# Performance work log

Hardware: AMD Instinct MI355X
Metric: run time of the kernel (lower is better)

Reference implementation:

```python
import jax, jax.numpy as jnp
import numpy as np

B, T = 8, 30000
DIM = 3
HID = 128          # hidden_dim
CD = 128           # c_dim
R = 64             # plane_resolution
NB = 5             # n_blocks


def setup_inputs() -> dict:
    key = jax.random.key(0)
    ks = jax.random.split(key, 10)
    points = jax.random.uniform(ks[0], (B, T, DIM), dtype=jnp.float32)
    index_xz = jax.random.randint(ks[1], (B, T), 0, R * R, dtype=jnp.int32)
    index_xy = jax.random.randint(ks[2], (B, T), 0, R * R, dtype=jnp.int32)
    index_yz = jax.random.randint(ks[3], (B, T), 0, R * R, dtype=jnp.int32)
    s_in = 1.0 / np.sqrt(DIM)
    s_h2 = 1.0 / np.sqrt(2 * HID)
    s_h = 1.0 / np.sqrt(HID)
    fc_pos_w = jax.random.normal(ks[4], (DIM, 2 * HID), jnp.float32) * s_in
    fc_pos_b = jnp.zeros((2 * HID,), jnp.float32)
    fc0_w = jax.random.normal(ks[5], (NB, 2 * HID, HID), jnp.float32) * s_h2
    fc0_b = jnp.zeros((NB, HID), jnp.float32)
    fc1_w = jax.random.normal(ks[6], (NB, HID, HID), jnp.float32) * s_h
    fc1_b = jnp.zeros((NB, HID), jnp.float32)
    sc_w = jax.random.normal(ks[7], (NB, 2 * HID, HID), jnp.float32) * s_h2
    fc_c_w = jax.random.normal(ks[8], (HID, CD), jnp.float32) * s_h
    fc_c_b = jnp.zeros((CD,), jnp.float32)
    return dict(points=points, index_xz=index_xz, index_xy=index_xy, index_yz=index_yz,
                fc_pos_w=fc_pos_w, fc_pos_b=fc_pos_b, fc0_w=fc0_w, fc0_b=fc0_b,
                fc1_w=fc1_w, fc1_b=fc1_b, sc_w=sc_w, fc_c_w=fc_c_w, fc_c_b=fc_c_b)


def _resnet_block(x, w0, b0, w1, b1, ws):
    # ResnetBlockFC: fc_0(relu(x)) -> fc_1(relu(net)); shortcut is bias-free Linear
    net = jax.nn.relu(x) @ w0 + b0
    dx = jax.nn.relu(net) @ w1 + b1
    return x @ ws + dx


def _pool_max_gather(feat, idx):
    # scatter_max per batch into R*R bins, then gather back per-point
    def per(f, i):  # f: [T, C], i: [T]
        seg = jax.ops.segment_max(f, i, num_segments=R * R)  # [R2, C]
        return seg[i]
    return jax.vmap(per)(feat, idx)


def _plane_mean(c, idx):
    # scatter_mean of c [B, T, CD] into [B, CD, R, R] plane features
    def per(f, i):
        s = jax.ops.segment_sum(f, i, num_segments=R * R)  # [R2, CD]
        cnt = jax.ops.segment_sum(jnp.ones((f.shape[0],), f.dtype), i, num_segments=R * R)
        return s / jnp.maximum(cnt, 1.0)[:, None]
    m = jax.vmap(per)(c, idx)  # [B, R2, CD]
    return jnp.transpose(m, (0, 2, 1)).reshape(c.shape[0], CD, R, R)


def reference(points, index_xz, index_xy, index_yz, fc_pos_w, fc_pos_b,
              fc0_w, fc0_b, fc1_w, fc1_b, sc_w, fc_c_w, fc_c_b):
    idxs = (index_xz, index_xy, index_yz)
    net = points @ fc_pos_w + fc_pos_b                    # [B, T, 2*HID]
    net = _resnet_block(net, fc0_w[0], fc0_b[0], fc1_w[0], fc1_b[0], sc_w[0])  # [B, T, HID]
    for i in range(1, NB):
        pooled = sum(_pool_max_gather(net, idx) for idx in idxs)  # pool_local sums over plane keys
        net = jnp.concatenate([net, pooled], axis=2)      # [B, T, 2*HID]
        net = _resnet_block(net, fc0_w[i], fc0_b[i], fc1_w[i], fc1_b[i], sc_w[i])
    c = net @ fc_c_w + fc_c_b                             # [B, T, CD]
    # fea dict {'xz','xy','yz'} returned as a stacked array [3, B, CD, R, R]
    return jnp.stack([_plane_mean(c, index_xz), _plane_mean(c, index_xy), _plane_mean(c, index_yz)], axis=0)
```

## Files before the change

### kernel.cpp

```cpp
#include <hip/hip_runtime.h>
#include <float.h>

#define BATCH 8
#define TPTS 30000
#define NPR 30016
#define HID 128
#define R2 4096
#define NPTS (BATCH * TPTS)
#define PB 64
#define XS 264
#define HS 136

typedef __attribute__((ext_vector_type(8))) short short8;
typedef __attribute__((ext_vector_type(4))) short short4v;
typedef __attribute__((ext_vector_type(4))) float f32x4;

__device__ __forceinline__ short f2bf(float f) {
    unsigned u = __float_as_uint(f);
    u += 0x7fff + ((u >> 16) & 1);
    return (short)(u >> 16);
}
__device__ __forceinline__ float bf2f(unsigned short u) {
    return __uint_as_float(((unsigned)u) << 16);
}
__device__ __forceinline__ unsigned relu2(unsigned u) {
    unsigned sm = u & 0x80008000u;
    unsigned d  = sm - (sm >> 15);
    return u & ~d;
}
__device__ __forceinline__ short8 relu8(short8 v) {
    union { short8 s; unsigned u[4]; } a;
    a.s = v;
#pragma unroll
    for (int i = 0; i < 4; ++i) a.u[i] = relu2(a.u[i]);
    return a.s;
}

__global__ void k_fill4(float4* p, float v, int n4) {
    int i = blockIdx.x * blockDim.x + threadIdx.x;
    if (i < n4) p[i] = make_float4(v, v, v, v);
}

__global__ __launch_bounds__(256) void k_prep(
    const float* __restrict__ fc0w, const float* __restrict__ fc1w, const float* __restrict__ scw,
    const float* __restrict__ fccw,
    short* __restrict__ Wt0, short* __restrict__ Wts, short* __restrict__ Wt1,
    short* __restrict__ Wtc)
{
    int i = blockIdx.x * 256 + threadIdx.x;
    if (i < 5 * 128 * 256) {
        int r = i >> 15;
        int c = (i >> 8) & 127;
        int k = i & 255;
        Wt0[i] = f2bf(fc0w[(r * 256 + k) * 128 + c]);
        Wts[i] = f2bf(scw [(r * 256 + k) * 128 + c]);
    }
    if (i < 5 * 128 * 128) {
        int r = i >> 14;
        int c = (i >> 7) & 127;
        int k = i & 127;
        Wt1[i] = f2bf(fc1w[(r * 128 + k) * 128 + c]);
    }
    if (i < 128 * 128) {
        int c = (i >> 7) & 127;
        int k = i & 127;
        Wtc[i] = f2bf(fccw[k * 128 + c]);
    }
}

__global__ void k_hist(const int* __restrict__ i0, const int* __restrict__ i1,
                       const int* __restrict__ i2, int* __restrict__ hist)
{
    int t = blockIdx.x * 256 + threadIdx.x;
    if (t >= NPTS) return;
    int b = t / TPTS;
    atomicAdd(&hist[(0 * BATCH + b) * R2 + i0[t]], 1);
    atomicAdd(&hist[(1 * BATCH + b) * R2 + i1[t]], 1);
    atomicAdd(&hist[(2 * BATCH + b) * R2 + i2[t]], 1);
}

__global__ __launch_bounds__(256) void k_scan(const int* __restrict__ hist,
                                              int* __restrict__ starts, int* __restrict__ cursor)
{
    int pb = blockIdx.x;
    const int* h = hist + pb * R2;
    int tid = threadIdx.x;
    __shared__ int part[257];
    int loc[16]; int s = 0;
    int base = tid * 16;
#pragma unroll
    for (int q = 0; q < 16; ++q) { loc[q] = s; s += h[base + q]; }
    part[tid + 1] = s;
    __syncthreads();
    if (tid == 0) {
        part[0] = 0;
        for (int i = 1; i <= 256; ++i) part[i] += part[i - 1];
    }
    __syncthreads();
    int off = part[tid];
#pragma unroll
    for (int q = 0; q < 16; ++q) {
        int v = off + loc[q];
        starts[pb * 4097 + base + q] = v;
        cursor[pb * R2 + base + q] = v;
    }
    if (tid == 255) starts[pb * 4097 + 4096] = part[256];
}

__global__ void k_scatter(const int* __restrict__ i0, const int* __restrict__ i1,
                          const int* __restrict__ i2, int* __restrict__ cursor,
                          unsigned short* __restrict__ order)
{
    int t = blockIdx.x * 256 + threadIdx.x;
    if (t >= NPTS) return;
    int b = t / TPTS;
    int tt = t - b * TPTS;
    int s0 = atomicAdd(&cursor[(0 * BATCH + b) * R2 + i0[t]], 1);
    order[(0 * BATCH + b) * TPTS + s0] = (unsigned short)tt;
    int s1 = atomicAdd(&cursor[(1 * BATCH + b) * R2 + i1[t]], 1);
    order[(1 * BATCH + b) * TPTS + s1] = (unsigned short)tt;
    int s2 = atomicAdd(&cursor[(2 * BATCH + b) * R2 + i2[t]], 1);
    order[(2 * BATCH + b) * TPTS + s2] = (unsigned short)tt;
}

__global__ __launch_bounds__(256) void k_poolmax(
    const short* __restrict__ net, const int* __restrict__ starts,
    const unsigned short* __restrict__ order, short* __restrict__ seg)
{
    int b = blockIdx.x;
    int plane = blockIdx.y >> 10;
    int bin = (blockIdx.y & 1023) * 4 + (threadIdx.x >> 6);
    int pb = plane * BATCH + b;
    int lane = threadIdx.x & 63;
    int s = starts[pb * 4097 + bin], e = starts[pb * 4097 + bin + 1];
    if (s == e) return;
    const unsigned short* ord = order + pb * TPTS;
    float vx = -FLT_MAX, vy = -FLT_MAX;
    for (int i = s; i < e; ++i) {
        int t = b * NPR + ord[i];
        unsigned u = *(const unsigned*)(net + t * HID + lane * 2);
        vx = fmaxf(vx, bf2f((unsigned short)(u & 0xFFFF)));
        vy = fmaxf(vy, bf2f((unsigned short)(u >> 16)));
    }
    unsigned o = ((unsigned short)f2bf(vx)) | (((unsigned)(unsigned short)f2bf(vy)) << 16);
    *(unsigned*)(seg + (pb * R2 + bin) * HID + lane * 2) = o;
}

__global__ __launch_bounds__(256) void k_poolmean(
    const short* __restrict__ net, const int* __restrict__ starts,
    const unsigned short* __restrict__ order, short* __restrict__ meanb)
{
    int b = blockIdx.x;
    int plane = blockIdx.y >> 10;
    int bin = (blockIdx.y & 1023) * 4 + (threadIdx.x >> 6);
    int pb = plane * BATCH + b;
    int lane = threadIdx.x & 63;
    int s = starts[pb * 4097 + bin], e = starts[pb * 4097 + bin + 1];
    const unsigned short* ord = order + pb * TPTS;
    float vx = 0.f, vy = 0.f;
    for (int i = s; i < e; ++i) {
        int t = b * NPR + ord[i];
        unsigned u = *(const unsigned*)(net + t * HID + lane * 2);
        vx += bf2f((unsigned short)(u & 0xFFFF));
        vy += bf2f((unsigned short)(u >> 16));
    }
    float inv = 1.f / fmaxf((float)(e - s), 1.f);
    unsigned o = ((unsigned short)f2bf(vx * inv)) | (((unsigned)(unsigned short)f2bf(vy * inv)) << 16);
    *(unsigned*)(meanb + (pb * R2 + bin) * HID + lane * 2) = o;
}

__device__ __forceinline__ void resnet_body(
    short* xs, const float* b0s, const float* b1s,
    const short* __restrict__ Wt0r, const short* __restrict__ Wtsr,
    const short* __restrict__ Wt1r, short* __restrict__ net_out, int t0)
{
    int tid = threadIdx.x;
    int lane = tid & 63;
    int wave = tid >> 6;
    int n    = lane & 15;
    int quad = lane >> 4;
    int ch0  = wave * 32;

    f32x4 accS[2][4] = {};
    f32x4 accF[2][4] = {};
    for (int ks = 0; ks < 8; ++ks) {
        int ko = ks * 32 + quad * 8;
        short8 aS[2], aF[2];
#pragma unroll
        for (int c = 0; c < 2; ++c) {
            int row = ch0 + c * 16 + n;
            aS[c] = *(const short8*)(Wtsr + row * 256 + ko);
            aF[c] = *(const short8*)(Wt0r + row * 256 + ko);
        }
#pragma unroll
        for (int p = 0; p < 4; ++p) {
            short8 bX = *(const short8*)(xs + (p * 16 + n) * XS + ko);
            short8 bR = relu8(bX);
#pragma unroll
            for (int c = 0; c < 2; ++c) {
                accS[c][p] = __builtin_amdgcn_mfma_f32_16x16x32_bf16(aS[c], bX, accS[c][p], 0, 0, 0);
                accF[c][p] = __builtin_amdgcn_mfma_f32_16x16x32_bf16(aF[c], bR, accF[c][p], 0, 0, 0);
            }
        }
    }
    __syncthreads();

    short* h = xs;
#pragma unroll
    for (int c = 0; c < 2; ++c) {
        int chb = ch0 + c * 16 + quad * 4;
#pragma unroll
        for (int p = 0; p < 4; ++p) {
            int pt = p * 16 + n;
            short4v hv;
#pragma unroll
            for (int r = 0; r < 4; ++r)
                hv[r] = f2bf(fmaxf(accF[c][p][r] + b0s[chb + r], 0.f));
            *(short4v*)&h[pt * HS + chb] = hv;
        }
    }
    __syncthreads();

    for (int ks = 0; ks < 4; ++ks) {
        int ko = ks * 32 + quad * 8;
        short8 a1[2];
#pragma unroll
        for (int c = 0; c < 2; ++c)
            a1[c] = *(const short8*)(Wt1r + (ch0 + c * 16 + n) * 128 + ko);
#pragma unroll
        for (int p = 0; p < 4; ++p) {
            short8 bh = *(const short8*)&h[(p * 16 + n) * HS + ko];
#pragma unroll
            for (int c = 0; c < 2; ++c)
                accS[c][p] = __builtin_amdgcn_mfma_f32_16x16x32_bf16(a1[c], bh, accS[c][p], 0, 0, 0);
        }
    }
    __syncthreads();

#pragma unroll
    for (int c = 0; c < 2; ++c) {
        int chb = ch0 + c * 16 + quad * 4;
#pragma unroll
        for (int p = 0; p < 4; ++p) {
            int pt = p * 16 + n;
            short4v o;
#pragma unroll
            for (int r = 0; r < 4; ++r)
                o[r] = f2bf(accS[c][p][r] + b1s[chb + r]);
            *(short4v*)&h[pt * HS + chb] = o;
        }
    }
    __syncthreads();

    int pr = tid >> 4, l8 = (tid & 15) * 8;
#pragma unroll
    for (int it = 0; it < 4; ++it) {
        int p = it * 16 + pr;
        *(short8*)(net_out + (t0 + p) * HID + l8) = *(const short8*)&h[p * HS + l8];
    }
}

__global__ __launch_bounds__(256, 4) void k_mblock0(
    const float* __restrict__ pts, const float* __restrict__ Wp, const float* __restrict__ bp,
    const short* __restrict__ Wt0, const short* __restrict__ Wts, const short* __restrict__ Wt1,
    const float* __restrict__ b0, const float* __restrict__ b1, short* __restrict__ net)
{
    __shared__ short xs[PB * XS];
    __shared__ float b0s[HID], b1s[HID];
    int tid = threadIdx.x;
    int b  = blockIdx.x;
    int r0 = blockIdx.y * PB;
    if (tid < 128) { b0s[tid] = b0[tid]; b1s[tid] = b1[tid]; }

    int j = tid & 127, half = tid >> 7;
    int col = half * 128 + j;
    float w0 = Wp[col], w1 = Wp[256 + col], w2 = Wp[512 + col];
    float bb = bp[col];
    for (int p = 0; p < PB; ++p) {
        int tt = r0 + p; if (tt > TPTS - 1) tt = TPTS - 1;
        const float* pp = pts + (b * TPTS + tt) * 3;
        float v = fmaf(pp[2], w2, fmaf(pp[1], w1, fmaf(pp[0], w0, bb)));
        xs[p * XS + col] = f2bf(v);
    }
    __syncthreads();
    resnet_body(xs, b0s, b1s, Wt0, Wts, Wt1, net, b * NPR + r0);
}

__global__ __launch_bounds__(256, 4) void k_mblock(
    const short* __restrict__ net_in, const short* __restrict__ seg,
    const int* __restrict__ i0, const int* __restrict__ i1, const int* __restrict__ i2,
    const short* __restrict__ Wt0, const short* __restrict__ Wts, const short* __restrict__ Wt1,
    const float* __restrict__ b0, const float* __restrict__ b1, short* __restrict__ net_out)
{
    __shared__ short xs[PB * XS];
    __shared__ float b0s[HID], b1s[HID];
    int tid = threadIdx.x;
    int b  = blockIdx.x;
    int r0 = blockIdx.y * PB;
    if (tid < 128) { b0s[tid] = b0[tid]; b1s[tid] = b1[tid]; }

    int pr = tid >> 4;
    int l8 = (tid & 15) * 8;
#pragma unroll
    for (int it = 0; it < 4; ++it) {
        int p = it * 16 + pr;
        int tt = r0 + p;
        int ttc = tt > TPTS - 1 ? TPTS - 1 : tt;
        int ib = b * TPTS + ttc;
        int a0 = i0[ib], a1 = i1[ib], a2 = i2[ib];
        *(short8*)&xs[p * XS + l8] = *(const short8*)(net_in + (b * NPR + tt) * HID + l8);
        short8 s0 = *(const short8*)(seg + ((0 * BATCH + b) * R2 + a0) * HID + l8);
        short8 s1 = *(const short8*)(seg + ((1 * BATCH + b) * R2 + a1) * HID + l8);
        short8 s2 = *(const short8*)(seg + ((2 * BATCH + b) * R2 + a2) * HID + l8);
        short8 pv;
#pragma unroll
        for (int r = 0; r < 8; ++r)
            pv[r] = f2bf(bf2f((unsigned short)s0[r]) + bf2f((unsigned short)s1[r]) + bf2f((unsigned short)s2[r]));
        *(short8*)&xs[p * XS + 128 + l8] = pv;
    }
    __syncthreads();
    resnet_body(xs, b0s, b1s, Wt0, Wts, Wt1, net_out, b * NPR + r0);
}

__global__ __launch_bounds__(256) void k_gemmout(
    const short* __restrict__ meanb, const short* __restrict__ Wtc, const float* __restrict__ bc,
    const int* __restrict__ starts, float* __restrict__ out)
{
    __shared__ short bs[64 * HS];
    __shared__ float tile[128 * 66];
    __shared__ float bcs[HID];
    __shared__ int   flg[64];
    int tid = threadIdx.x;
    int b = blockIdx.x;
    int plane = blockIdx.y >> 6;
    int pb = plane * BATCH + b;
    int bin0 = (blockIdx.y & 63) * 64;

    if (tid < 128) bcs[tid] = bc[tid];
    if (tid < 64)  flg[tid] = (starts[pb * 4097 + bin0 + tid + 1] > starts[pb * 4097 + bin0 + tid]);
    for (int c8 = tid; c8 < 1024; c8 += 256) {
        int p = c8 >> 4, l = (c8 & 15) * 8;
        *(short8*)&bs[p * HS + l] = *(const short8*)(meanb + (pb * R2 + bin0 + p) * HID + l);
    }
    __syncthreads();

    int lane = tid & 63, wave = tid >> 6;
    int n = lane & 15, quad = lane >> 4;
    int ch0 = wave * 32;
    f32x4 acc[2][4] = {};
    for (int ks = 0; ks < 4; ++ks) {
        int ko = ks * 32 + quad * 8;
        short8 a[2];
#pragma unroll
        for (int c = 0; c < 2; ++c)
            a[c] = *(const short8*)(Wtc + (ch0 + c * 16 + n) * 128 + ko);
#pragma unroll
        for (int p = 0; p < 4; ++p) {
            short8 bh = *(const short8*)&bs[(p * 16 + n) * HS + ko];
#pragma unroll
            for (int c = 0; c < 2; ++c)
                acc[c][p] = __builtin_amdgcn_mfma_f32_16x16x32_bf16(a[c], bh, acc[c][p], 0, 0, 0);
        }
    }
#pragma unroll
    for (int c = 0; c < 2; ++c) {
        int chb = ch0 + c * 16 + quad * 4;
#pragma unroll
        for (int p = 0; p < 4; ++p) {
            int bin = p * 16 + n;
#pragma unroll
            for (int r = 0; r < 4; ++r)
                tile[(chb + r) * 66 + bin] = acc[c][p][r] + bcs[chb + r];
        }
    }
    __syncthreads();

    for (int c4 = tid; c4 < 2048; c4 += 256) {
        int ch = c4 >> 4, b4 = (c4 & 15) * 4;
        float4 o;
        o.x = flg[b4 + 0] ? tile[ch * 66 + b4 + 0] : 0.f;
        o.y = flg[b4 + 1] ? tile[ch * 66 + b4 + 1] : 0.f;
        o.z = flg[b4 + 2] ? tile[ch * 66 + b4 + 2] : 0.f;
        o.w = flg[b4 + 3] ? tile[ch * 66 + b4 + 3] : 0.f;
        *(float4*)(out + (pb * 128 + ch) * R2 + bin0 + b4) = o;
    }
}

extern "C" void kernel_launch(void* const* d_in, const int* in_sizes, int n_in,
                              void* d_out, int out_size, void* d_ws, size_t ws_size,
                              hipStream_t stream) {
    const float* pts  = (const float*)d_in[0];
    const int*   ixz  = (const int*)d_in[1];
    const int*   ixy  = (const int*)d_in[2];
    const int*   iyz  = (const int*)d_in[3];
    const float* Wp   = (const float*)d_in[4];
    const float* bp   = (const float*)d_in[5];
    const float* fc0w = (const float*)d_in[6];
    const float* fc0b = (const float*)d_in[7];
    const float* fc1w = (const float*)d_in[8];
    const float* fc1b = (const float*)d_in[9];
    const float* scw  = (const float*)d_in[10];
    const float* Wc   = (const float*)d_in[11];
    const float* bc   = (const float*)d_in[12];
    float* out = (float*)d_out;

    short* Wt0 = (short*)d_ws;
    short* Wts = Wt0 + 163840;
    short* Wt1 = Wts + 163840;
    short* Wtc = Wt1 + 81920;
    short* net  = Wtc + 16384;
    short* segb = net + 30736384;
    int* hist   = (int*)(segb + 12582912);
    int* starts = hist + 98304;
    unsigned short* order = (unsigned short*)(starts + 98328);

    k_prep<<<dim3(640), 256, 0, stream>>>(fc0w, fc1w, scw, Wc, Wt0, Wts, Wt1, Wtc);
    k_fill4<<<dim3(96), 256, 0, stream>>>((float4*)hist, 0.f, 98304 / 4);
    k_hist<<<dim3((NPTS + 255) / 256), 256, 0, stream>>>(ixz, ixy, iyz, hist);
    k_scan<<<dim3(24), 256, 0, stream>>>(hist, starts, hist);
    k_scatter<<<dim3((NPTS + 255) / 256), 256, 0, stream>>>(ixz, ixy, iyz, hist, order);

    k_mblock0<<<dim3(8, NPR / PB), 256, 0, stream>>>(pts, Wp, bp, Wt0, Wts, Wt1, fc0b, fc1b, net);

    for (int r = 1; r < 5; ++r) {
        k_poolmax<<<dim3(8, 3 * R2 / 4), 256, 0, stream>>>(net, starts, order, segb);
        k_mblock<<<dim3(8, NPR / PB), 256, 0, stream>>>(
            net, segb, ixz, ixy, iyz,
            Wt0 + r * 32768, Wts + r * 32768, Wt1 + r * 16384,
            fc0b + r * 128, fc1b + r * 128, net);
    }

    k_poolmean<<<dim3(8, 3 * R2 / 4), 256, 0, stream>>>(net, starts, order, segb);
    k_gemmout<<<dim3(8, 3 * 64), 256, 0, stream>>>(segb, Wtc, bc, starts, out);
}
```

Baseline: 993.0 us.

## Use 512-thread blocks in resnet kernels with 16 channels per wave

The fused resnet block kernels now launch 512 threads, so each of 8 waves computes 16 output channels instead of 4 waves computing 32. This halves the accumulator registers per thread and adds waves to hide the weight and gather load latency. The fc_pos prologue is also rewritten so each thread computes one point's 32 columns and writes them with vector stores, and the index loads in the gather are hoisted ahead of the data loads. In exchange, each wave does less MFMA work per LDS B-fragment load, and the per-block barriers cover twice as many waves.

```diff
diff --git a/kernel.cpp b/kernel.cpp
--- a/kernel.cpp
+++ b/kernel.cpp
@@ -179,43 +179,35 @@
     int wave = tid >> 6;
     int n    = lane & 15;
     int quad = lane >> 4;
-    int ch0  = wave * 32;
-
-    f32x4 accS[2][4] = {};
-    f32x4 accF[2][4] = {};
+    int ch0  = wave * 16;
+
+    f32x4 accS[4] = {};
+    f32x4 accF[4] = {};
     for (int ks = 0; ks < 8; ++ks) {
         int ko = ks * 32 + quad * 8;
-        short8 aS[2], aF[2];
-#pragma unroll
-        for (int c = 0; c < 2; ++c) {
-            int row = ch0 + c * 16 + n;
-            aS[c] = *(const short8*)(Wtsr + row * 256 + ko);
-            aF[c] = *(const short8*)(Wt0r + row * 256 + ko);
-        }
+        int row = ch0 + n;
+        short8 aS = *(const short8*)(Wtsr + row * 256 + ko);
+        short8 aF = *(const short8*)(Wt0r + row * 256 + ko);
 #pragma unroll
         for (int p = 0; p < 4; ++p) {
             short8 bX = *(const short8*)(xs + (p * 16 + n) * XS + ko);
             short8 bR = relu8(bX);
-#pragma unroll
-            for (int c = 0; c < 2; ++c) {
-                accS[c][p] = __builtin_amdgcn_mfma_f32_16x16x32_bf16(aS[c], bX, accS[c][p], 0, 0, 0);
-                accF[c][p] = __builtin_amdgcn_mfma_f32_16x16x32_bf16(aF[c], bR, accF[c][p], 0, 0, 0);
-            }
+            accS[p] = __builtin_amdgcn_mfma_f32_16x16x32_bf16(aS, bX, accS[p], 0, 0, 0);
+            accF[p] = __builtin_amdgcn_mfma_f32_16x16x32_bf16(aF, bR, accF[p], 0, 0, 0);
         }
     }
     __syncthreads();
 
     short* h = xs;
-#pragma unroll
-    for (int c = 0; c < 2; ++c) {
-        int chb = ch0 + c * 16 + quad * 4;
+    {
+        int chb = ch0 + quad * 4;
 #pragma unroll
         for (int p = 0; p < 4; ++p) {
             int pt = p * 16 + n;
             short4v hv;
 #pragma unroll
             for (int r = 0; r < 4; ++r)
-                hv[r] = f2bf(fmaxf(accF[c][p][r] + b0s[chb + r], 0.f));
+                hv[r] = f2bf(fmaxf(accF[p][r] + b0s[chb + r], 0.f));
             *(short4v*)&h[pt * HS + chb] = hv;
         }
     }
@@ -223,30 +215,24 @@
 
     for (int ks = 0; ks < 4; ++ks) {
         int ko = ks * 32 + quad * 8;
-        short8 a1[2];
-#pragma unroll
-        for (int c = 0; c < 2; ++c)
-            a1[c] = *(const short8*)(Wt1r + (ch0 + c * 16 + n) * 128 + ko);
+        short8 a1 = *(const short8*)(Wt1r + (ch0 + n) * 128 + ko);
 #pragma unroll
         for (int p = 0; p < 4; ++p) {
             short8 bh = *(const short8*)&h[(p * 16 + n) * HS + ko];
-#pragma unroll
-            for (int c = 0; c < 2; ++c)
-                accS[c][p] = __builtin_amdgcn_mfma_f32_16x16x32_bf16(a1[c], bh, accS[c][p], 0, 0, 0);
-        }
-    }
-    __syncthreads();
-
-#pragma unroll
-    for (int c = 0; c < 2; ++c) {
-        int chb = ch0 + c * 16 + quad * 4;
+            accS[p] = __builtin_amdgcn_mfma_f32_16x16x32_bf16(a1, bh, accS[p], 0, 0, 0);
+        }
+    }
+    __syncthreads();
+
+    {
+        int chb = ch0 + quad * 4;
 #pragma unroll
         for (int p = 0; p < 4; ++p) {
             int pt = p * 16 + n;
             short4v o;
 #pragma unroll
             for (int r = 0; r < 4; ++r)
-                o[r] = f2bf(accS[c][p][r] + b1s[chb + r]);
+                o[r] = f2bf(accS[p][r] + b1s[chb + r]);
             *(short4v*)&h[pt * HS + chb] = o;
         }
     }
@@ -254,13 +240,13 @@
 
     int pr = tid >> 4, l8 = (tid & 15) * 8;
 #pragma unroll
-    for (int it = 0; it < 4; ++it) {
-        int p = it * 16 + pr;
+    for (int it = 0; it < 2; ++it) {
+        int p = it * 32 + pr;
         *(short8*)(net_out + (t0 + p) * HID + l8) = *(const short8*)&h[p * HS + l8];
     }
 }
 
-__global__ __launch_bounds__(256, 4) void k_mblock0(
+__global__ __launch_bounds__(512, 4) void k_mblock0(
     const float* __restrict__ pts, const float* __restrict__ Wp, const float* __restrict__ bp,
     const short* __restrict__ Wt0, const short* __restrict__ Wts, const short* __restrict__ Wt1,
     const float* __restrict__ b0, const float* __restrict__ b1, short* __restrict__ net)
@@ -272,21 +258,28 @@
     int r0 = blockIdx.y * PB;
     if (tid < 128) { b0s[tid] = b0[tid]; b1s[tid] = b1[tid]; }
 
-    int j = tid & 127, half = tid >> 7;
-    int col = half * 128 + j;
-    float w0 = Wp[col], w1 = Wp[256 + col], w2 = Wp[512 + col];
-    float bb = bp[col];
-    for (int p = 0; p < PB; ++p) {
-        int tt = r0 + p; if (tt > TPTS - 1) tt = TPTS - 1;
-        const float* pp = pts + (b * TPTS + tt) * 3;
-        float v = fmaf(pp[2], w2, fmaf(pp[1], w1, fmaf(pp[0], w0, bb)));
-        xs[p * XS + col] = f2bf(v);
+    int pt = tid >> 3;
+    int sub = tid & 7;
+    int tt = r0 + pt; if (tt > TPTS - 1) tt = TPTS - 1;
+    const float* pp = pts + (b * TPTS + tt) * 3;
+    float px = pp[0], py = pp[1], pz = pp[2];
+#pragma unroll
+    for (int c8 = 0; c8 < 4; ++c8) {
+        int col0 = sub * 32 + c8 * 8;
+        short8 v8;
+#pragma unroll
+        for (int r = 0; r < 8; ++r) {
+            int col = col0 + r;
+            float v = fmaf(pz, Wp[512 + col], fmaf(py, Wp[256 + col], fmaf(px, Wp[col], bp[col])));
+            v8[r] = f2bf(v);
+        }
+        *(short8*)&xs[pt * XS + col0] = v8;
     }
     __syncthreads();
     resnet_body(xs, b0s, b1s, Wt0, Wts, Wt1, net, b * NPR + r0);
 }
 
-__global__ __launch_bounds__(256, 4) void k_mblock(
+__global__ __launch_bounds__(512, 4) void k_mblock(
     const short* __restrict__ net_in, const short* __restrict__ seg,
     const int* __restrict__ i0, const int* __restrict__ i1, const int* __restrict__ i2,
     const short* __restrict__ Wt0, const short* __restrict__ Wts, const short* __restrict__ Wt1,
@@ -301,17 +294,22 @@
 
     int pr = tid >> 4;
     int l8 = (tid & 15) * 8;
-#pragma unroll
-    for (int it = 0; it < 4; ++it) {
-        int p = it * 16 + pr;
-        int tt = r0 + p;
+    int a0[2], a1[2], a2[2];
+#pragma unroll
+    for (int it = 0; it < 2; ++it) {
+        int tt = r0 + it * 32 + pr;
         int ttc = tt > TPTS - 1 ? TPTS - 1 : tt;
         int ib = b * TPTS + ttc;
-        int a0 = i0[ib], a1 = i1[ib], a2 = i2[ib];
+        a0[it] = i0[ib]; a1[it] = i1[ib]; a2[it] = i2[ib];
+    }
+#pragma unroll
+    for (int it = 0; it < 2; ++it) {
+        int p = it * 32 + pr;
+        int tt = r0 + p;
         *(short8*)&xs[p * XS + l8] = *(const short8*)(net_in + (b * NPR + tt) * HID + l8);
-        short8 s0 = *(const short8*)(seg + ((0 * BATCH + b) * R2 + a0) * HID + l8);
-        short8 s1 = *(const short8*)(seg + ((1 * BATCH + b) * R2 + a1) * HID + l8);
-        short8 s2 = *(const short8*)(seg + ((2 * BATCH + b) * R2 + a2) * HID + l8);
+        short8 s0 = *(const short8*)(seg + ((0 * BATCH + b) * R2 + a0[it]) * HID + l8);
+        short8 s1 = *(const short8*)(seg + ((1 * BATCH + b) * R2 + a1[it]) * HID + l8);
+        short8 s2 = *(const short8*)(seg + ((2 * BATCH + b) * R2 + a2[it]) * HID + l8);
         short8 pv;
 #pragma unroll
         for (int r = 0; r < 8; ++r)
@@ -420,11 +418,11 @@
     k_scan<<<dim3(24), 256, 0, stream>>>(hist, starts, hist);
     k_scatter<<<dim3((NPTS + 255) / 256), 256, 0, stream>>>(ixz, ixy, iyz, hist, order);
 
-    k_mblock0<<<dim3(8, NPR / PB), 256, 0, stream>>>(pts, Wp, bp, Wt0, Wts, Wt1, fc0b, fc1b, net);
+    k_mblock0<<<dim3(8, NPR / PB), 512, 0, stream>>>(pts, Wp, bp, Wt0, Wts, Wt1, fc0b, fc1b, net);
 
     for (int r = 1; r < 5; ++r) {
         k_poolmax<<<dim3(8, 3 * R2 / 4), 256, 0, stream>>>(net, starts, order, segb);
-        k_mblock<<<dim3(8, NPR / PB), 256, 0, stream>>>(
+        k_mblock<<<dim3(8, NPR / PB), 512, 0, stream>>>(
             net, segb, ixz, ixy, iyz,
             Wt0 + r * 32768, Wts + r * 32768, Wt1 + r * 16384,
             fc0b + r * 128, fc1b + r * 128, net);
```

Measured after the change: 1.092 ms. 9.9% more time.
